# Performance work log

Measured on AMD Instinct MI355X. Metric: run time of the kernel, lower is better.

## Reference

```python
import jax, jax.numpy as jnp
import numpy as np

NUM_USER = 200000
NUM_QUESTION = 20000
NUM_CONCEPT = 128
DIM_HIDDEN = 512
BATCH = 16384


def _build_graph():
    # Deterministic DAG: edges go from lower to higher concept index, so
    # topological order is 0..C-1. Edge list is ordered by (to, from), so the
    # predecessors of node k occupy a contiguous slice of edge indices, matching
    # know_graph[know_graph['to']==k].sort_values(by='from').index.
    rng = np.random.RandomState(0)
    preds, offs, e = [], [], 0
    for k in range(NUM_CONCEPT):
        lp = 0 if k == 0 else int(rng.randint(0, min(k, 3) + 1))
        p = sorted(rng.choice(k, size=lp, replace=False).tolist()) if lp > 0 else []
        preds.append(p)
        offs.append(e)
        e += lp
    return preds, offs, e

PREDS, OFFS, NUM_EDGE = _build_graph()


def setup_inputs() -> dict:
    key = jax.random.key(0)
    ks = jax.random.split(key, 16)
    h2 = max(DIM_HIDDEN // 2, 1)
    inp = {
        'user_id': jax.random.randint(ks[0], (BATCH,), 0, NUM_USER),
        'question_id': jax.random.randint(ks[1], (BATCH,), 0, NUM_QUESTION),
        'priori': jax.random.normal(ks[2], (NUM_USER, NUM_CONCEPT), jnp.float32) * 0.1,
        'condi_p': jax.random.normal(ks[3], (NUM_USER, NUM_EDGE), jnp.float32) * 0.1,
        'condi_n': jax.random.normal(ks[4], (NUM_USER, NUM_EDGE), jnp.float32) * 0.1,
        'item_diff': jax.random.normal(ks[5], (NUM_QUESTION, NUM_CONCEPT), jnp.float32) * 0.1,
        'item_disc': jax.random.normal(ks[6], (NUM_QUESTION, 1), jnp.float32) * 0.1,
        'q_table': (jax.random.uniform(ks[7], (NUM_QUESTION, NUM_CONCEPT)) < 0.1).astype(jnp.float32),
        'Wu': jax.random.normal(ks[8], (DIM_HIDDEN, NUM_CONCEPT), jnp.float32) * 0.05,
        'bu': jnp.zeros((DIM_HIDDEN,), jnp.float32),
        'Wi': jax.random.normal(ks[9], (DIM_HIDDEN, NUM_CONCEPT), jnp.float32) * 0.05,
        'bi': jnp.zeros((DIM_HIDDEN,), jnp.float32),
        'W1': jax.random.normal(ks[10], (h2, DIM_HIDDEN), jnp.float32) * 0.05,
        'b1': jnp.zeros((h2,), jnp.float32),
        'W2': jax.random.normal(ks[11], (1, h2), jnp.float32) * 0.05,
        'b2': jnp.zeros((1,), jnp.float32),
    }
    return inp


def _posterior(user_id, priori, condi_p, condi_n):
    bp = jax.nn.sigmoid(priori[user_id])   # [B, C]
    bcp = jax.nn.sigmoid(condi_p[user_id])  # [B, E]
    bcn = jax.nn.sigmoid(condi_n[user_id])  # [B, E]
    post = [None] * NUM_CONCEPT
    for k in range(NUM_CONCEPT):
        preds = PREDS[k]
        lp = len(preds)
        if lp == 0:
            post[k] = bp[:, k]
            continue
        pr = jnp.stack([post[p] for p in preds], axis=1)          # [B, lp]
        cp = bcp[:, OFFS[k]:OFFS[k] + lp] ** (1.0 / lp)           # [B, lp]
        cn = bcn[:, OFFS[k]:OFFS[k] + lp] ** (1.0 / lp)
        # Exact closed form of the 2^lp mask sum: sum over binary masks of
        # prod_j(m_j*cp_j*pr_j + (1-m_j)*cn_j*(1-pr_j)) = prod_j(cp_j*pr_j + cn_j*(1-pr_j))
        post[k] = jnp.prod(cp * pr + cn * (1.0 - pr), axis=1)
    return jnp.stack(post, axis=1)  # [B, C]


def reference(user_id, question_id, priori, condi_p, condi_n, item_diff, item_disc,
              q_table, Wu, bu, Wi, bi, W1, b1, W2, b2):
    user_mastery = _posterior(user_id, priori, condi_p, condi_n)      # [B, C]
    diff = jax.nn.sigmoid(item_diff[question_id])                     # [B, C]
    disc = jax.nn.sigmoid(item_disc[question_id])                     # [B, 1]
    q = q_table[question_id]                                          # [B, C]
    user_factor = jnp.tanh((user_mastery * q) @ Wu.T + bu)            # [B, H]
    item_factor = jax.nn.sigmoid((diff * q) @ Wi.T + bi)              # [B, H]
    x = (user_factor - item_factor) * disc
    x = jax.nn.sigmoid(x @ W1.T + b1)
    x = jax.nn.sigmoid(x @ W2.T + b2)                                 # [B, 1]
    return jnp.squeeze(x, axis=-1)
```

## Files before the change

### kernel.cpp

```cpp
#include <hip/hip_runtime.h>
#include <hip/hip_bf16.h>
#include <stdint.h>

typedef __hip_bfloat16 bf16;

struct GraphArg {
  short offs[128];
  unsigned char lp[128];
  unsigned char preds[384];
};

namespace {
struct HostMT {
  uint32_t mt[624]; int pos;
  void seed(uint32_t s){
    mt[0]=s;
    for(int i=1;i<624;i++) mt[i]=1812433253u*(mt[i-1]^(mt[i-1]>>30))+(uint32_t)i;
    pos=624;
  }
  uint32_t next(){
    if(pos>=624){
      for(int i=0;i<624;i++){
        uint32_t y=(mt[i]&0x80000000u)|(mt[(i+1)%624]&0x7fffffffu);
        mt[i]=mt[(i+397)%624]^(y>>1)^((y&1u)?0x9908b0dfu:0u);
      }
      pos=0;
    }
    uint32_t y=mt[pos++];
    y^=y>>11; y^=(y<<7)&0x9d2c5680u; y^=(y<<15)&0xefc60000u; y^=y>>18;
    return y;
  }
  uint64_t next64(){ uint64_t hi=next(); uint64_t lo=next(); return (hi<<32)|lo; }
  uint32_t masked32(uint32_t rng){
    if(!rng) return 0u;
    uint32_t mask=rng; mask|=mask>>1; mask|=mask>>2; mask|=mask>>4; mask|=mask>>8; mask|=mask>>16;
    uint32_t v; do{ v=next()&mask; }while(v>rng); return v;
  }
  uint64_t masked64(uint64_t rng){
    if(!rng) return 0ull;
    uint64_t mask=rng; mask|=mask>>1; mask|=mask>>2; mask|=mask>>4; mask|=mask>>8; mask|=mask>>16; mask|=mask>>32;
    uint64_t v; do{ v=next64()&mask; }while(v>rng); return v;
  }
};

int build_graph(GraphArg& g, bool rand64, bool shuf64){
  HostMT st; st.seed(0u);
  int e=0; int perm[128];
  for(int k=0;k<128;k++){
    int l=0;
    if(k>0){
      uint32_t rng=(uint32_t)(k<3?k:3);
      l = rand64 ? (int)st.masked64(rng) : (int)st.masked32(rng);
    }
    g.offs[k]=(short)e; g.lp[k]=(unsigned char)l;
    g.preds[k*3]=0; g.preds[k*3+1]=0; g.preds[k*3+2]=0;
    if(l>0){
      for(int i=0;i<k;i++) perm[i]=i;
      for(int i=k-1;i>=1;i--){
        uint32_t j = shuf64 ? (uint32_t)st.masked64((uint64_t)i) : st.masked32((uint32_t)i);
        int t=perm[i]; perm[i]=perm[j]; perm[j]=t;
      }
      int sel[3]; for(int j=0;j<l;j++) sel[j]=perm[j];
      for(int a=1;a<l;a++){ int v=sel[a]; int b=a-1; while(b>=0&&sel[b]>v){sel[b+1]=sel[b];b--;} sel[b+1]=v; }
      for(int j=0;j<l;j++) g.preds[k*3+j]=(unsigned char)sel[j];
    }
    e+=l;
  }
  return e;
}
}

__device__ __forceinline__ float bf2f(bf16 v){ return __bfloat162float(v); }
__device__ __forceinline__ float sigmoidf_(float x){ return 1.0f/(1.0f+expf(-x)); }

template<bool F32> __device__ __forceinline__ float ld1(const void* p, long long i){
  if constexpr(F32) return ((const float*)p)[i];
  else return bf2f(((const bf16*)p)[i]);
}
template<bool F32> __device__ __forceinline__ void ld8(const void* p, long long i, float* f){
  if constexpr(F32){
    const float4* q = (const float4*)((const float*)p + i);
    float4 a=q[0], b=q[1];
    f[0]=a.x; f[1]=a.y; f[2]=a.z; f[3]=a.w; f[4]=b.x; f[5]=b.y; f[6]=b.z; f[7]=b.w;
  } else {
    union { uint4 u; unsigned short s[8]; } x;
    x.u = *reinterpret_cast<const uint4*>((const bf16*)p + i);
#pragma unroll
    for(int j=0;j<8;j++){ unsigned uu=((unsigned)x.s[j])<<16; float ff; __builtin_memcpy(&ff,&uu,4); f[j]=ff; }
  }
}
template<bool F32> __device__ __forceinline__ void st1(void* p, long long i, float v){
  if constexpr(F32) ((float*)p)[i]=v;
  else ((bf16*)p)[i]=__float2bfloat16(v);
}

template<bool F32>
__global__ __launch_bounds__(256) void fused(
    const int* __restrict__ user_id, const int* __restrict__ question_id,
    const void* __restrict__ priori, const void* __restrict__ condi_p, const void* __restrict__ condi_n,
    const void* __restrict__ item_diff, const void* __restrict__ item_disc, const void* __restrict__ q_table,
    const void* __restrict__ Wu, const void* __restrict__ bu,
    const void* __restrict__ Wi, const void* __restrict__ bi,
    const void* __restrict__ W1, const void* __restrict__ b1,
    const void* __restrict__ W2, const void* __restrict__ b2,
    void* __restrict__ out, long long E, long long maxCondi, GraphArg g)
{
  {
    const unsigned short* ph = (const unsigned short*)priori;
    int cnt=0;
#pragma unroll
    for(int i=0;i<64;i++){ unsigned ex=(ph[i]>>7)&0xFFu; cnt += (ex>=0x82u)?1:0; }
    const bool isF32 = (cnt>=4);
    if(isF32 != F32) return;
  }

  __shared__ char uA[24704];
  __shared__ float s_mq[32*128];
  __shared__ float s_dq[32*128];
  float* s_post=(float*)uA;
  float* s_x   =(float*)uA;
  float* s_x1  =(float*)(uA+16384);
  float* s_disc=(float*)(uA+24576);

  const int tid=threadIdx.x;
  const long long b0=(long long)blockIdx.x*32;

  if(tid<32){
    const int u=user_id[b0+tid];
    const long long ubase=(long long)u*E;
    for(int k=0;k<128;k++){
      const int lp=(int)g.lp[k];
      float pk;
      if(lp==0){
        pk=sigmoidf_(ld1<F32>(priori,(long long)u*128+k));
      } else {
        const int off=(int)g.offs[k];
        float prod=1.0f;
        for(int j=0;j<lp;j++){
          long long idx=ubase+off+j; if(idx>maxCondi) idx=maxCondi;
          float bcp=sigmoidf_(ld1<F32>(condi_p,idx));
          float bcn=sigmoidf_(ld1<F32>(condi_n,idx));
          float cp,cn;
          if(lp==1){cp=bcp;cn=bcn;}
          else if(lp==2){cp=sqrtf(bcp);cn=sqrtf(bcn);}
          else {cp=cbrtf(bcp);cn=cbrtf(bcn);}
          float pr=s_post[(int)g.preds[k*3+j]*32+tid];
          prod*=cp*pr+cn*(1.0f-pr);
        }
        pk=prod;
      }
      s_post[k*32+tid]=pk;
    }
  }
  __syncthreads();

  for(int i=tid;i<32*128;i+=256){
    const int e=i>>7, c=i&127;
    const int q=question_id[b0+e];
    const float qv=ld1<F32>(q_table,(long long)q*128+c);
    s_mq[i]=s_post[c*32+e]*qv;
    s_dq[i]=sigmoidf_(ld1<F32>(item_diff,(long long)q*128+c))*qv;
    if(c==0) s_disc[e]=sigmoidf_(ld1<F32>(item_disc,q));
  }
  __syncthreads();

  for(int tile=0;tile<4;tile++){
    const int e0=tile*8;
    for(int half=0;half<2;half++){
      const int o=tid+half*256;
      float aU[8],aI[8];
#pragma unroll
      for(int e=0;e<8;e++){aU[e]=0.0f;aI[e]=0.0f;}
      for(int c=0;c<128;c+=8){
        float u8[8],i8[8];
        ld8<F32>(Wu,(long long)o*128+c,u8);
        ld8<F32>(Wi,(long long)o*128+c,i8);
#pragma unroll
        for(int e=0;e<8;e++){
          const float* m=&s_mq[(e0+e)*128+c];
          const float* d=&s_dq[(e0+e)*128+c];
#pragma unroll
          for(int j=0;j<8;j++){ aU[e]+=u8[j]*m[j]; aI[e]+=i8[j]*d[j]; }
        }
      }
      const float bou=ld1<F32>(bu,o), boi=ld1<F32>(bi,o);
#pragma unroll
      for(int e=0;e<8;e++){
        float uf=tanhf(aU[e]+bou);
        float fi=sigmoidf_(aI[e]+boi);
        s_x[e*512+o]=(uf-fi)*s_disc[e0+e];
      }
    }
    __syncthreads();
    {
      float a[8];
#pragma unroll
      for(int e=0;e<8;e++) a[e]=0.0f;
      for(int c=0;c<512;c+=8){
        float w8[8]; ld8<F32>(W1,(long long)tid*512+c,w8);
#pragma unroll
        for(int e=0;e<8;e++){
          const float* x=&s_x[e*512+c];
#pragma unroll
          for(int j=0;j<8;j++) a[e]+=w8[j]*x[j];
        }
      }
      const float bb=ld1<F32>(b1,tid);
#pragma unroll
      for(int e=0;e<8;e++) s_x1[e*256+tid]=sigmoidf_(a[e]+bb);
    }
    __syncthreads();
    {
      const int e=tid>>5, l=tid&31;
      float a=0.0f;
      for(int h=l;h<256;h+=32) a+=s_x1[e*256+h]*ld1<F32>(W2,h);
      for(int off=16;off>0;off>>=1) a+=__shfl_down(a,off,32);
      if(l==0) st1<F32>(out,b0+e0+e,sigmoidf_(a+ld1<F32>(b2,0)));
    }
    __syncthreads();
  }
}

extern "C" void kernel_launch(void* const* d_in, const int* in_sizes, int n_in,
                              void* d_out, int out_size, void* d_ws, size_t ws_size,
                              hipStream_t stream) {
  const int* user_id     = (const int*)d_in[0];
  const int* question_id = (const int*)d_in[1];
  const void* priori     = d_in[2];
  const void* condi_p    = d_in[3];
  const void* condi_n    = d_in[4];
  const void* item_diff  = d_in[5];
  const void* item_disc  = d_in[6];
  const void* q_table    = d_in[7];
  const void* Wu = d_in[8];  const void* bu = d_in[9];
  const void* Wi = d_in[10]; const void* bi = d_in[11];
  const void* W1 = d_in[12]; const void* b1 = d_in[13];
  const void* W2 = d_in[14]; const void* b2 = d_in[15];
  (void)n_in; (void)out_size; (void)d_ws; (void)ws_size;

  const int batch    = in_sizes[0];
  const int num_user = in_sizes[2] / 128;
  const long long E  = in_sizes[3] / num_user;
  const long long maxCondi = (long long)num_user * E - 1;

  GraphArg g;
  int e_tot = build_graph(g, false, false);
  if(e_tot != (int)E) e_tot = build_graph(g, true,  false);
  if(e_tot != (int)E) e_tot = build_graph(g, false, true);
  if(e_tot != (int)E) e_tot = build_graph(g, true,  true);
  if(e_tot != (int)E) (void)build_graph(g, false, false);

  const int blocks = batch / 32;
  fused<false><<<blocks,256,0,stream>>>(user_id,question_id,priori,condi_p,condi_n,
      item_diff,item_disc,q_table,Wu,bu,Wi,bi,W1,b1,W2,b2,d_out,E,maxCondi,g);
  fused<true ><<<blocks,256,0,stream>>>(user_id,question_id,priori,condi_p,condi_n,
      item_diff,item_disc,q_table,Wu,bu,Wi,bi,W1,b1,W2,b2,d_out,E,maxCondi,g);
}
```

Measured before the change: 755.3 us.

## Parallelize posterior edge loads across block and widen block to 512 threads

All threads now cooperatively prefetch the sigmoid priors and the transformed conditional edge probabilities (sigmoid plus root by predecessor count) into shared memory. Only the serial product over the topological order stays on 32 threads. This removes the long dependent global-load chain in the single-wavefront posterior phase. The block grows to 512 threads so each thread owns one hidden unit, and the shared-memory reads become float4 with a padded posterior layout. The larger shared arena (~58KB) and 512-thread blocks may reduce occupancy, and the staged path only applies when the edge count is at most 165.

```diff
diff --git a/kernel.cpp b/kernel.cpp
--- a/kernel.cpp
+++ b/kernel.cpp
@@ -8,6 +8,7 @@
   short offs[128];
   unsigned char lp[128];
   unsigned char preds[384];
+  unsigned char elp[384];
 };
 
 namespace {
@@ -45,6 +46,7 @@
 
 int build_graph(GraphArg& g, bool rand64, bool shuf64){
   HostMT st; st.seed(0u);
+  for(int j=0;j<384;j++) g.elp[j]=0;
   int e=0; int perm[128];
   for(int k=0;k<128;k++){
     int l=0;
@@ -62,7 +64,7 @@
       }
       int sel[3]; for(int j=0;j<l;j++) sel[j]=perm[j];
       for(int a=1;a<l;a++){ int v=sel[a]; int b=a-1; while(b>=0&&sel[b]>v){sel[b+1]=sel[b];b--;} sel[b+1]=v; }
-      for(int j=0;j<l;j++) g.preds[k*3+j]=(unsigned char)sel[j];
+      for(int j=0;j<l;j++){ g.preds[k*3+j]=(unsigned char)sel[j]; g.elp[e+j]=(unsigned char)l; }
     }
     e+=l;
   }
@@ -95,7 +97,7 @@
 }
 
 template<bool F32>
-__global__ __launch_bounds__(256) void fused(
+__global__ __launch_bounds__(512,4) void fused(
     const int* __restrict__ user_id, const int* __restrict__ question_id,
     const void* __restrict__ priori, const void* __restrict__ condi_p, const void* __restrict__ condi_n,
     const void* __restrict__ item_diff, const void* __restrict__ item_disc, const void* __restrict__ q_table,
@@ -114,26 +116,65 @@
     if(isF32 != F32) return;
   }
 
-  __shared__ char uA[24704];
-  __shared__ float s_mq[32*128];
-  __shared__ float s_dq[32*128];
-  float* s_post=(float*)uA;
-  float* s_x   =(float*)uA;
-  float* s_x1  =(float*)(uA+16384);
-  float* s_disc=(float*)(uA+24576);
+  __shared__ __align__(16) char arena[59264];
+  float* s_cp  =(float*)(arena);
+  float* s_cn  =(float*)(arena+21120);
+  float* s_post=(float*)(arena+42240);
+  float* s_mq  =(float*)(arena);
+  float* s_dq  =(float*)(arena+16384);
+  float* s_x   =(float*)(arena+32768);
+  float* s_x1  =(float*)(arena+49152);
+  float* s_disc=(float*)(arena+59136);
 
   const int tid=threadIdx.x;
   const long long b0=(long long)blockIdx.x*32;
+  const bool staged = (E<=165);
+
+  for(int i=tid;i<32*128;i+=512){
+    const int e=i>>7, k=i&127;
+    const int u=user_id[b0+e];
+    s_post[k*33+e]=sigmoidf_(ld1<F32>(priori,(long long)u*128+k));
+  }
+  if(staged){
+    const int j=tid&255, eh=tid>>8;
+    for(int p=0;p<16;p++){
+      const int e=p*2+eh;
+      if((long long)j<E){
+        const int u=user_id[b0+e];
+        const long long idx=(long long)u*E+j;
+        const int lp=(int)g.elp[j];
+        float cp=sigmoidf_(ld1<F32>(condi_p,idx));
+        float cn=sigmoidf_(ld1<F32>(condi_n,idx));
+        if(lp==2){cp=sqrtf(cp);cn=sqrtf(cn);}
+        else if(lp==3){cp=cbrtf(cp);cn=cbrtf(cn);}
+        s_cp[e*165+j]=cp; s_cn[e*165+j]=cn;
+      }
+    }
+  }
+  __syncthreads();
 
   if(tid<32){
-    const int u=user_id[b0+tid];
-    const long long ubase=(long long)u*E;
-    for(int k=0;k<128;k++){
-      const int lp=(int)g.lp[k];
-      float pk;
-      if(lp==0){
-        pk=sigmoidf_(ld1<F32>(priori,(long long)u*128+k));
-      } else {
+    const int e=tid;
+    if(staged){
+      for(int k=0;k<128;k++){
+        const int lp=(int)g.lp[k];
+        if(lp==0) continue;
+        const int off=(int)g.offs[k];
+        float prod=1.0f;
+        for(int j=0;j<lp;j++){
+          const float pr=s_post[(int)g.preds[k*3+j]*33+e];
+          const float cp=s_cp[e*165+off+j];
+          const float cn=s_cn[e*165+off+j];
+          prod*=cp*pr+cn*(1.0f-pr);
+        }
+        s_post[k*33+e]=prod;
+      }
+    } else {
+      const int u=user_id[b0+e];
+      const long long ubase=(long long)u*E;
+      for(int k=0;k<128;k++){
+        const int lp=(int)g.lp[k];
+        if(lp==0) continue;
         const int off=(int)g.offs[k];
         float prod=1.0f;
         for(int j=0;j<lp;j++){
@@ -144,30 +185,29 @@
           if(lp==1){cp=bcp;cn=bcn;}
           else if(lp==2){cp=sqrtf(bcp);cn=sqrtf(bcn);}
           else {cp=cbrtf(bcp);cn=cbrtf(bcn);}
-          float pr=s_post[(int)g.preds[k*3+j]*32+tid];
+          const float pr=s_post[(int)g.preds[k*3+j]*33+e];
           prod*=cp*pr+cn*(1.0f-pr);
         }
-        pk=prod;
-      }
-      s_post[k*32+tid]=pk;
+        s_post[k*33+e]=prod;
+      }
     }
   }
   __syncthreads();
 
-  for(int i=tid;i<32*128;i+=256){
+  for(int i=tid;i<32*128;i+=512){
     const int e=i>>7, c=i&127;
     const int q=question_id[b0+e];
     const float qv=ld1<F32>(q_table,(long long)q*128+c);
-    s_mq[i]=s_post[c*32+e]*qv;
-    s_dq[i]=sigmoidf_(ld1<F32>(item_diff,(long long)q*128+c))*qv;
+    s_mq[e*128+c]=s_post[c*33+e]*qv;
+    s_dq[e*128+c]=sigmoidf_(ld1<F32>(item_diff,(long long)q*128+c))*qv;
     if(c==0) s_disc[e]=sigmoidf_(ld1<F32>(item_disc,q));
   }
   __syncthreads();
 
   for(int tile=0;tile<4;tile++){
     const int e0=tile*8;
-    for(int half=0;half<2;half++){
-      const int o=tid+half*256;
+    {
+      const int o=tid;
       float aU[8],aI[8];
 #pragma unroll
       for(int e=0;e<8;e++){aU[e]=0.0f;aI[e]=0.0f;}
@@ -177,44 +217,46 @@
         ld8<F32>(Wi,(long long)o*128+c,i8);
 #pragma unroll
         for(int e=0;e<8;e++){
-          const float* m=&s_mq[(e0+e)*128+c];
-          const float* d=&s_dq[(e0+e)*128+c];
-#pragma unroll
-          for(int j=0;j<8;j++){ aU[e]+=u8[j]*m[j]; aI[e]+=i8[j]*d[j]; }
+          const float4* m4=(const float4*)&s_mq[(e0+e)*128+c];
+          const float4* d4=(const float4*)&s_dq[(e0+e)*128+c];
+          const float4 ma=m4[0], mb=m4[1], da=d4[0], db=d4[1];
+          const float mf[8]={ma.x,ma.y,ma.z,ma.w,mb.x,mb.y,mb.z,mb.w};
+          const float df[8]={da.x,da.y,da.z,da.w,db.x,db.y,db.z,db.w};
+#pragma unroll
+          for(int j=0;j<8;j++){ aU[e]+=u8[j]*mf[j]; aI[e]+=i8[j]*df[j]; }
         }
       }
       const float bou=ld1<F32>(bu,o), boi=ld1<F32>(bi,o);
 #pragma unroll
-      for(int e=0;e<8;e++){
-        float uf=tanhf(aU[e]+bou);
-        float fi=sigmoidf_(aI[e]+boi);
-        s_x[e*512+o]=(uf-fi)*s_disc[e0+e];
-      }
+      for(int e=0;e<8;e++)
+        s_x[e*512+o]=(tanhf(aU[e]+bou)-sigmoidf_(aI[e]+boi))*s_disc[e0+e];
     }
     __syncthreads();
     {
-      float a[8];
-#pragma unroll
-      for(int e=0;e<8;e++) a[e]=0.0f;
+      const int o=tid&255, h=tid>>8;
+      float a[4]={0.0f,0.0f,0.0f,0.0f};
       for(int c=0;c<512;c+=8){
-        float w8[8]; ld8<F32>(W1,(long long)tid*512+c,w8);
-#pragma unroll
-        for(int e=0;e<8;e++){
-          const float* x=&s_x[e*512+c];
-#pragma unroll
-          for(int j=0;j<8;j++) a[e]+=w8[j]*x[j];
+        float w8[8]; ld8<F32>(W1,(long long)o*512+c,w8);
+#pragma unroll
+        for(int e=0;e<4;e++){
+          const float4* x4=(const float4*)&s_x[(h*4+e)*512+c];
+          const float4 xa=x4[0], xb=x4[1];
+          const float xf[8]={xa.x,xa.y,xa.z,xa.w,xb.x,xb.y,xb.z,xb.w};
+#pragma unroll
+          for(int j=0;j<8;j++) a[e]+=w8[j]*xf[j];
         }
       }
-      const float bb=ld1<F32>(b1,tid);
-#pragma unroll
-      for(int e=0;e<8;e++) s_x1[e*256+tid]=sigmoidf_(a[e]+bb);
+      const float bb=ld1<F32>(b1,o);
+#pragma unroll
+      for(int e=0;e<4;e++) s_x1[(h*4+e)*256+o]=sigmoidf_(a[e]+bb);
     }
     __syncthreads();
     {
-      const int e=tid>>5, l=tid&31;
+      const int e=tid>>6, l=tid&63;
       float a=0.0f;
-      for(int h=l;h<256;h+=32) a+=s_x1[e*256+h]*ld1<F32>(W2,h);
-      for(int off=16;off>0;off>>=1) a+=__shfl_down(a,off,32);
+      for(int hh=l;hh<256;hh+=64) a+=s_x1[e*256+hh]*ld1<F32>(W2,hh);
+#pragma unroll
+      for(int off=32;off>0;off>>=1) a+=__shfl_down(a,off,64);
       if(l==0) st1<F32>(out,b0+e0+e,sigmoidf_(a+ld1<F32>(b2,0)));
     }
     __syncthreads();
@@ -251,8 +293,8 @@
   if(e_tot != (int)E) (void)build_graph(g, false, false);
 
   const int blocks = batch / 32;
-  fused<false><<<blocks,256,0,stream>>>(user_id,question_id,priori,condi_p,condi_n,
+  fused<false><<<blocks,512,0,stream>>>(user_id,question_id,priori,condi_p,condi_n,
       item_diff,item_disc,q_table,Wu,bu,Wi,bi,W1,b1,W2,b2,d_out,E,maxCondi,g);
-  fused<true ><<<blocks,256,0,stream>>>(user_id,question_id,priori,condi_p,condi_n,
+  fused<true ><<<blocks,512,0,stream>>>(user_id,question_id,priori,condi_p,condi_n,
       item_diff,item_disc,q_table,Wu,bu,Wi,bi,W1,b1,W2,b2,d_out,E,maxCondi,g);
 }
```

Measured after the change: 855.5 us. 13.3% more time.

## Parallelize posterior edge loads across threads and halve per-block batch

Applied to the files above, without the earlier changes.

Priori sigmoids and the per-edge conditional sigmoids and roots are now computed by all threads cooperatively into shared memory, instead of 32 threads walking the whole DAG serially with global loads. The sequential DAG recurrence then only reads from shared memory, uses an XOR-swizzled layout to avoid bank conflicts, and skips nodes without predecessors. Blocks now cover 16 samples instead of 32, so there are twice as many blocks but Wu/Wi/W1 are reloaded per block more often. Edge staging only applies when the edge count fits the shared buffer; otherwise it falls back to the old per-thread global path.

```diff
diff --git a/kernel.cpp b/kernel.cpp
--- a/kernel.cpp
+++ b/kernel.cpp
@@ -8,6 +8,7 @@
   short offs[128];
   unsigned char lp[128];
   unsigned char preds[384];
+  unsigned char elp[384];
 };
 
 namespace {
@@ -45,6 +46,7 @@
 
 int build_graph(GraphArg& g, bool rand64, bool shuf64){
   HostMT st; st.seed(0u);
+  for(int j=0;j<384;j++) g.elp[j]=0;
   int e=0; int perm[128];
   for(int k=0;k<128;k++){
     int l=0;
@@ -62,7 +64,7 @@
       }
       int sel[3]; for(int j=0;j<l;j++) sel[j]=perm[j];
       for(int a=1;a<l;a++){ int v=sel[a]; int b=a-1; while(b>=0&&sel[b]>v){sel[b+1]=sel[b];b--;} sel[b+1]=v; }
-      for(int j=0;j<l;j++) g.preds[k*3+j]=(unsigned char)sel[j];
+      for(int j=0;j<l;j++){ g.preds[k*3+j]=(unsigned char)sel[j]; g.elp[e+j]=(unsigned char)l; }
     }
     e+=l;
   }
@@ -93,6 +95,8 @@
   if constexpr(F32) ((float*)p)[i]=v;
   else ((bf16*)p)[i]=__float2bfloat16(v);
 }
+
+__device__ __forceinline__ int pidx(int k,int e){ return (k<<4) + (e ^ (k&15)); }
 
 template<bool F32>
 __global__ __launch_bounds__(256) void fused(
@@ -114,26 +118,66 @@
     if(isF32 != F32) return;
   }
 
-  __shared__ char uA[24704];
-  __shared__ float s_mq[32*128];
-  __shared__ float s_dq[32*128];
-  float* s_post=(float*)uA;
-  float* s_x   =(float*)uA;
-  float* s_x1  =(float*)(uA+16384);
-  float* s_disc=(float*)(uA+24576);
+  __shared__ __align__(16) char arena[40960];
+  float* s_dq  =(float*)(arena);
+  float* s_post=(float*)(arena+8192);
+  float* s_cp  =(float*)(arena+16384);
+  float* s_cn  =(float*)(arena+26880);
+  float* s_mq  =(float*)(arena+16384);
+  float* s_x   =(float*)(arena+24576);
+  float* s_x1  =(float*)(arena+8192);
 
   const int tid=threadIdx.x;
-  const long long b0=(long long)blockIdx.x*32;
-
-  if(tid<32){
-    const int u=user_id[b0+tid];
-    const long long ubase=(long long)u*E;
-    for(int k=0;k<128;k++){
-      const int lp=(int)g.lp[k];
-      float pk;
-      if(lp==0){
-        pk=sigmoidf_(ld1<F32>(priori,(long long)u*128+k));
-      } else {
+  const long long b0=(long long)blockIdx.x*16;
+  const int Ei=(int)E;
+  const bool staged=(Ei>0 && Ei<=164);
+
+  float qv[8];
+#pragma unroll
+  for(int it=0;it<8;++it){
+    const int i=tid+(it<<8);
+    const int e=i>>7, c=i&127;
+    const int u=user_id[b0+e];
+    s_post[pidx(c,e)]=sigmoidf_(ld1<F32>(priori,(long long)u*128+c));
+    const int q=question_id[b0+e];
+    const float qvv=ld1<F32>(q_table,(long long)q*128+c);
+    qv[it]=qvv;
+    s_dq[e*128+c]=sigmoidf_(ld1<F32>(item_diff,(long long)q*128+c))*qvv;
+  }
+  if(staged && tid<Ei){
+    const int j=tid, lp=(int)g.elp[j];
+    for(int e=0;e<16;e++){
+      const int u=user_id[b0+e];
+      const long long idx=(long long)u*E+j;
+      float cp=sigmoidf_(ld1<F32>(condi_p,idx));
+      float cn=sigmoidf_(ld1<F32>(condi_n,idx));
+      if(lp==2){cp=sqrtf(cp);cn=sqrtf(cn);}
+      else if(lp==3){cp=cbrtf(cp);cn=cbrtf(cn);}
+      s_cp[e*Ei+j]=cp; s_cn[e*Ei+j]=cn;
+    }
+  }
+  __syncthreads();
+
+  if(tid<16){
+    const int e=tid;
+    if(staged){
+      for(int k=0;k<128;k++){
+        const int lp=(int)g.lp[k];
+        if(lp==0) continue;
+        const int off=(int)g.offs[k];
+        float prod=1.0f;
+        for(int j=0;j<lp;j++){
+          const float pr=s_post[pidx((int)g.preds[k*3+j],e)];
+          prod*=s_cp[e*Ei+off+j]*pr + s_cn[e*Ei+off+j]*(1.0f-pr);
+        }
+        s_post[pidx(k,e)]=prod;
+      }
+    } else {
+      const int u=user_id[b0+e];
+      const long long ubase=(long long)u*E;
+      for(int k=0;k<128;k++){
+        const int lp=(int)g.lp[k];
+        if(lp==0) continue;
         const int off=(int)g.offs[k];
         float prod=1.0f;
         for(int j=0;j<lp;j++){
@@ -144,28 +188,31 @@
           if(lp==1){cp=bcp;cn=bcn;}
           else if(lp==2){cp=sqrtf(bcp);cn=sqrtf(bcn);}
           else {cp=cbrtf(bcp);cn=cbrtf(bcn);}
-          float pr=s_post[(int)g.preds[k*3+j]*32+tid];
+          const float pr=s_post[pidx((int)g.preds[k*3+j],e)];
           prod*=cp*pr+cn*(1.0f-pr);
         }
-        pk=prod;
-      }
-      s_post[k*32+tid]=pk;
+        s_post[pidx(k,e)]=prod;
+      }
     }
   }
   __syncthreads();
 
-  for(int i=tid;i<32*128;i+=256){
+#pragma unroll
+  for(int it=0;it<8;++it){
+    const int i=tid+(it<<8);
     const int e=i>>7, c=i&127;
-    const int q=question_id[b0+e];
-    const float qv=ld1<F32>(q_table,(long long)q*128+c);
-    s_mq[i]=s_post[c*32+e]*qv;
-    s_dq[i]=sigmoidf_(ld1<F32>(item_diff,(long long)q*128+c))*qv;
-    if(c==0) s_disc[e]=sigmoidf_(ld1<F32>(item_disc,q));
+    s_mq[e*128+c]=s_post[pidx(c,e)]*qv[it];
   }
   __syncthreads();
 
-  for(int tile=0;tile<4;tile++){
+  for(int tile=0;tile<2;tile++){
     const int e0=tile*8;
+    float dsc[8];
+#pragma unroll
+    for(int e=0;e<8;e++){
+      const int q=question_id[b0+e0+e];
+      dsc[e]=sigmoidf_(ld1<F32>(item_disc,q));
+    }
     for(int half=0;half<2;half++){
       const int o=tid+half*256;
       float aU[8],aI[8];
@@ -188,7 +235,7 @@
       for(int e=0;e<8;e++){
         float uf=tanhf(aU[e]+bou);
         float fi=sigmoidf_(aI[e]+boi);
-        s_x[e*512+o]=(uf-fi)*s_disc[e0+e];
+        s_x[e*512+o]=(uf-fi)*dsc[e];
       }
     }
     __syncthreads();
@@ -250,7 +297,7 @@
   if(e_tot != (int)E) e_tot = build_graph(g, true,  true);
   if(e_tot != (int)E) (void)build_graph(g, false, false);
 
-  const int blocks = batch / 32;
+  const int blocks = batch / 16;
   fused<false><<<blocks,256,0,stream>>>(user_id,question_id,priori,condi_p,condi_n,
       item_diff,item_disc,q_table,Wu,bu,Wi,bi,W1,b1,W2,b2,d_out,E,maxCondi,g);
   fused<true ><<<blocks,256,0,stream>>>(user_id,question_id,priori,condi_p,condi_n,
```

Result: slower. 935.7 us (+23.9%).
